# Optimization experiments

Measured on AMD Instinct MI355X. Metric: run time of the kernel, lower is better.

Reference implementation:

```python
import jax, jax.numpy as jnp
import numpy as np

NUM_HEADS = 12


def setup_inputs() -> dict:
    key = jax.random.key(0)
    k0, k1, k2 = jax.random.split(key, 3)
    B, N, C = 32, 864, 768  # N = 2*t_h*t_w + s_h*s_w = 288 + 576
    x = jax.random.normal(k0, (B, N, C), dtype=jnp.float32)
    W_qkv = jax.random.normal(k1, (C, 3 * C), dtype=jnp.float32) * 0.02
    W_proj = jax.random.normal(k2, (C, C), dtype=jnp.float32) * 0.02
    b_proj = jnp.zeros((C,), dtype=jnp.float32)
    return {"x": x, "W_qkv": W_qkv, "W_proj": W_proj, "b_proj": b_proj,
            "t_h": 12, "t_w": 12, "s_h": 24, "s_w": 24}


def reference(x, W_qkv, W_proj, b_proj, t_h, t_w, s_h, s_w):
    B, N, C = x.shape
    H = NUM_HEADS
    d = C // H
    scale = d ** -0.5
    # qkv projection (no bias), shape [3, B, H, N, d]
    qkv = (x @ W_qkv).reshape(B, N, 3, H, d).transpose(2, 0, 3, 1, 4)
    q, k, v = qkv[0], qkv[1], qkv[2]
    Tt = 2 * t_h * t_w            # temporal (template) query tokens = 288
    Ts = s_h * s_w                # spatial (search) query tokens = 576
    Mt = 2 * ((t_h + 1) // 2) ** 2  # sub-sampled temporal kv tokens = 72
    Ms = (s_h * s_w) // 4           # sub-sampled spatial kv tokens = 144
    q_t, q_s = q[:, :, :Tt], q[:, :, Tt:Tt + Ts]
    k_t, k_s = k[:, :, :Mt], k[:, :, Mt:Mt + Ms]
    v_t, v_s = v[:, :, :Mt], v[:, :, Mt:Mt + Ms]
    # temporal queries attend spatial keys/values
    a_t = jax.nn.softmax(jnp.einsum('bhqd,bhkd->bhqk', q_t, k_s) * scale, axis=-1)
    x_t = jnp.einsum('bhqk,bhkd->bhqd', a_t, v_s).transpose(0, 2, 1, 3).reshape(B, Tt, C)
    # spatial queries attend temporal keys/values
    a_s = jax.nn.softmax(jnp.einsum('bhqd,bhkd->bhqk', q_s, k_t) * scale, axis=-1)
    x_s = jnp.einsum('bhqk,bhkd->bhqd', a_s, v_t).transpose(0, 2, 1, 3).reshape(B, Ts, C)
    out = jnp.concatenate([x_t, x_s], axis=1)  # [B, N, C]
    return out @ W_proj + b_proj
```

## Files before the change

kernel.cpp:

```cpp
#include <hip/hip_runtime.h>
#include <hip/hip_bf16.h>

typedef __attribute__((ext_vector_type(8))) short short8;
typedef __attribute__((ext_vector_type(4))) float floatx4;

#define MFMA16(a, b, c) __builtin_amdgcn_mfma_f32_16x16x32_bf16((a), (b), (c), 0, 0, 0)

static constexpr int Bb = 32, Nn = 864, Cc = 768, Hh = 12;
static constexpr int Mm = Bb * Nn;
static constexpr int NKV = 2 * Cc;
static constexpr int KVROWS = 256;

__device__ __forceinline__ void gload_lds16(const __hip_bfloat16* g, __hip_bfloat16* l) {
    __builtin_amdgcn_global_load_lds((const __attribute__((address_space(1))) void*)g,
                                     (__attribute__((address_space(3))) void*)l, 16, 0, 0);
}

static constexpr int CVT_BLKS = (Mm * Cc / 4) / 256;
static constexpr int TQKV_BLKS = (3 * Cc / 32) * (Cc / 32);
static constexpr int TPROJ_BLKS = (Cc / 32) * (Cc / 32);

__global__ __launch_bounds__(256) void prep_kernel(const float* __restrict__ x,
                                                   const float* __restrict__ Wqkv,
                                                   const float* __restrict__ Wproj,
                                                   __hip_bfloat16* __restrict__ xb,
                                                   __hip_bfloat16* __restrict__ WqkvT,
                                                   __hip_bfloat16* __restrict__ WprojT) {
    __shared__ float tile[32][33];
    const int bx = blockIdx.x;
    if (bx < CVT_BLKS) {
        const int i = bx * 256 + threadIdx.x;
        const float4 v = ((const float4*)x)[i];
        __hip_bfloat16 o[4] = {__float2bfloat16(v.x), __float2bfloat16(v.y),
                               __float2bfloat16(v.z), __float2bfloat16(v.w)};
        ((uint2*)xb)[i] = *(const uint2*)o;
        return;
    }
    const float* in;
    __hip_bfloat16* out;
    int R, C, bid;
    if (bx < CVT_BLKS + TQKV_BLKS) {
        bid = bx - CVT_BLKS; in = Wqkv; out = WqkvT; R = Cc; C = 3 * Cc;
    } else {
        bid = bx - CVT_BLKS - TQKV_BLKS; in = Wproj; out = WprojT; R = Cc; C = Cc;
    }
    const int c0 = (bid % (C / 32)) * 32, r0 = (bid / (C / 32)) * 32;
    const int tx = threadIdx.x & 31, ty = threadIdx.x >> 5;
#pragma unroll
    for (int i = 0; i < 32; i += 8)
        tile[ty + i][tx] = in[(size_t)(r0 + ty + i) * C + c0 + tx];
    __syncthreads();
#pragma unroll
    for (int i = 0; i < 32; i += 8)
        out[(size_t)(c0 + ty + i) * R + r0 + tx] = __float2bfloat16(tile[tx][ty + i]);
}

static constexpr int QBLKS = 6 * (Mm / 128);
static constexpr int KVBLKS = 12 * (Bb * KVROWS / 128);
static constexpr int QKV_NWG = QBLKS + KVBLKS;

__global__ __launch_bounds__(256) void gemm_qkv2(const __hip_bfloat16* __restrict__ A,
                                                 const __hip_bfloat16* __restrict__ WqkvT,
                                                 __hip_bfloat16* __restrict__ Qbuf,
                                                 __hip_bfloat16* __restrict__ KVbuf) {
    __shared__ __align__(16) __hip_bfloat16 As[8192];
    __shared__ __align__(16) __hip_bfloat16 Bs[8192];

    const int braw = (int)blockIdx.x;
    const int sid = (braw & 7) * (QKV_NWG / 8) + (braw >> 3);

    int arow0, orow0, btrow0, ncol0, Nout;
    __hip_bfloat16* Out;
    if (sid < QBLKS) {
        const int nt = sid % 6, mt = sid / 6;
        arow0 = mt * 128; orow0 = arow0;
        btrow0 = nt * 128; ncol0 = nt * 128;
        Out = Qbuf; Nout = Cc;
    } else {
        const int s = sid - QBLKS;
        const int nt = s % 12, mt = s / 12;
        const int bb = mt >> 1, keybase = (mt & 1) << 7;
        arow0 = bb * Nn + keybase;
        orow0 = bb * KVROWS + keybase;
        btrow0 = Cc + nt * 128;
        ncol0 = nt * 128;
        Out = KVbuf; Nout = NKV;
    }

    const int t = threadIdx.x;
    const int lane = t & 63, wave = t >> 6;
    const int wm = (wave >> 1) * 64, wn = (wave & 1) * 64;
    const int ln = lane & 15, quad = lane >> 4;

    floatx4 acc[4][4] = {};

    const int r0 = t >> 2;
    const int cst = (t & 3) * 8;
    const __hip_bfloat16* Ag = A + (size_t)(arow0 + r0) * Cc + cst;
    const __hip_bfloat16* Bg = WqkvT + (size_t)(btrow0 + r0) * Cc + cst;
    const size_t rowskip = (size_t)64 * Cc;

    for (int k0 = 0; k0 < Cc; k0 += 64) {
        gload_lds16(Ag + k0,                &As[t * 8]);
        gload_lds16(Ag + k0 + rowskip,      &As[2048 + t * 8]);
        gload_lds16(Ag + k0 + 32,           &As[4096 + t * 8]);
        gload_lds16(Ag + k0 + 32 + rowskip, &As[6144 + t * 8]);
        gload_lds16(Bg + k0,                &Bs[t * 8]);
        gload_lds16(Bg + k0 + rowskip,      &Bs[2048 + t * 8]);
        gload_lds16(Bg + k0 + 32,           &Bs[4096 + t * 8]);
        gload_lds16(Bg + k0 + 32 + rowskip, &Bs[6144 + t * 8]);
        __syncthreads();

#pragma unroll
        for (int s = 0; s < 2; s++) {
            short8 af[4], bfr[4];
#pragma unroll
            for (int i = 0; i < 4; i++)
                af[i] = *(const short8*)&As[s * 4096 + (wm + i * 16 + ln) * 32 + quad * 8];
#pragma unroll
            for (int j = 0; j < 4; j++)
                bfr[j] = *(const short8*)&Bs[s * 4096 + (wn + j * 16 + ln) * 32 + quad * 8];
#pragma unroll
            for (int i = 0; i < 4; i++)
#pragma unroll
                for (int j = 0; j < 4; j++)
                    acc[i][j] = MFMA16(af[i], bfr[j], acc[i][j]);
        }
        __syncthreads();
    }

#pragma unroll
    for (int j = 0; j < 4; j++) {
        const int n = ncol0 + wn + j * 16 + ln;
#pragma unroll
        for (int i = 0; i < 4; i++) {
            const int mrow = orow0 + wm + i * 16 + quad * 4;
#pragma unroll
            for (int r = 0; r < 4; r++)
                Out[(size_t)(mrow + r) * Nout + n] = __float2bfloat16(acc[i][j][r]);
        }
    }
}

__global__ __launch_bounds__(256) void gemm_proj(const __hip_bfloat16* __restrict__ A,
                                                 const __hip_bfloat16* __restrict__ BT,
                                                 float* __restrict__ Cout,
                                                 const float* __restrict__ bias) {
    __shared__ __align__(16) __hip_bfloat16 As[8192];
    __shared__ __align__(16) __hip_bfloat16 Bs[8192];
    const int gx = (int)gridDim.x;
    const int nwg = gx * (int)gridDim.y;
    const int braw = (int)blockIdx.y * gx + (int)blockIdx.x;
    const int sid = (braw & 7) * (nwg >> 3) + (braw >> 3);
    const int mt = sid / gx, nt = sid - mt * gx;
    const int m0 = mt << 7, n0 = nt * 128;
    const int t = threadIdx.x;
    const int lane = t & 63, wave = t >> 6;
    const int wm = (wave >> 1) * 64, wn = (wave & 1) * 64;
    const int ln = lane & 15, quad = lane >> 4;

    floatx4 acc[4][4] = {};
    const int r0 = t >> 2, cst = (t & 3) * 8;
    const __hip_bfloat16* Ag = A + (size_t)(m0 + r0) * Cc + cst;
    const __hip_bfloat16* Bg = BT + (size_t)(n0 + r0) * Cc + cst;
    const size_t rowskip = (size_t)64 * Cc;

    for (int k0 = 0; k0 < Cc; k0 += 64) {
        gload_lds16(Ag + k0,                &As[t * 8]);
        gload_lds16(Ag + k0 + rowskip,      &As[2048 + t * 8]);
        gload_lds16(Ag + k0 + 32,           &As[4096 + t * 8]);
        gload_lds16(Ag + k0 + 32 + rowskip, &As[6144 + t * 8]);
        gload_lds16(Bg + k0,                &Bs[t * 8]);
        gload_lds16(Bg + k0 + rowskip,      &Bs[2048 + t * 8]);
        gload_lds16(Bg + k0 + 32,           &Bs[4096 + t * 8]);
        gload_lds16(Bg + k0 + 32 + rowskip, &Bs[6144 + t * 8]);
        __syncthreads();
#pragma unroll
        for (int s = 0; s < 2; s++) {
            short8 af[4], bfr[4];
#pragma unroll
            for (int i = 0; i < 4; i++)
                af[i] = *(const short8*)&As[s * 4096 + (wm + i * 16 + ln) * 32 + quad * 8];
#pragma unroll
            for (int j = 0; j < 4; j++)
                bfr[j] = *(const short8*)&Bs[s * 4096 + (wn + j * 16 + ln) * 32 + quad * 8];
#pragma unroll
            for (int i = 0; i < 4; i++)
#pragma unroll
                for (int j = 0; j < 4; j++)
                    acc[i][j] = MFMA16(af[i], bfr[j], acc[i][j]);
        }
        __syncthreads();
    }
#pragma unroll
    for (int j = 0; j < 4; j++) {
        const int n = n0 + wn + j * 16 + ln;
        const float bv = bias[n];
#pragma unroll
        for (int i = 0; i < 4; i++) {
            const int mrow = m0 + wm + i * 16 + quad * 4;
#pragma unroll
            for (int r = 0; r < 4; r++)
                Cout[(size_t)(mrow + r) * Cc + n] = acc[i][j][r] + bv;
        }
    }
}

template <int L, int QOFF, int KVOFF, int NQT, int NCH>
__device__ __forceinline__ void attn_pair(const __hip_bfloat16* __restrict__ qb,
                                          const __hip_bfloat16* __restrict__ kv,
                                          __hip_bfloat16* __restrict__ attn,
                                          int qc, int h, int b,
                                          __hip_bfloat16* VTs) {
    constexpr int KPAD = NCH * 32;
    constexpr int VSTR = KPAD + 8;
    constexpr int NPAIR = NQT / 2;
    const int t = threadIdx.x, lane = t & 63, wave = t >> 6;
    const int ln = lane & 15, quad = lane >> 4;
    const __hip_bfloat16 z16 = __float2bfloat16(0.0f);

    const __hip_bfloat16* kbase = kv + (size_t)(b * KVROWS + KVOFF) * NKV + h * 64;
    const __hip_bfloat16* vbase = kbase + Cc;

    for (int c = t; c < KPAD * 8; c += 256) {
        const int key = c >> 3, s8 = c & 7, d0 = s8 * 8;
        const int colp = (key + 8 * s8) % KPAD;
        if (key < L) {
            uint4 raw = *(const uint4*)(vbase + (size_t)key * NKV + d0);
            const __hip_bfloat16* pv = (const __hip_bfloat16*)&raw;
#pragma unroll
            for (int jj = 0; jj < 8; jj++) VTs[(d0 + jj) * VSTR + colp] = pv[jj];
        } else {
#pragma unroll
            for (int jj = 0; jj < 8; jj++) VTs[(d0 + jj) * VSTR + colp] = z16;
        }
    }
    __syncthreads();

    const int pt = qc * 4 + wave;
    if (pt >= NPAIR) return;

    const int qt0 = 2 * pt;
    const __hip_bfloat16* qrowA =
        qb + (size_t)(b * Nn + QOFF + qt0 * 16 + ln) * Cc + h * 64;
    const __hip_bfloat16* qrowB = qrowA + (size_t)16 * Cc;
    const short8 aqA0 = *(const short8*)(qrowA + quad * 8);
    const short8 aqA1 = *(const short8*)(qrowA + 32 + quad * 8);
    const short8 aqB0 = *(const short8*)(qrowB + quad * 8);
    const short8 aqB1 = *(const short8*)(qrowB + 32 + quad * 8);

    float dsA = 0.0f, dsB = 0.0f;
    floatx4 accA[4] = {}, accB[4] = {};
    constexpr float CSC = 0.18033688011112042f;

#pragma unroll
    for (int ch = 0; ch < NCH; ch++) {
        unsigned int pkA[2][2], pkB[2][2];
#pragma unroll
        for (int ti2 = 0; ti2 < 2; ti2++) {
            const int ti = ch * 2 + ti2;
            if (ti * 16 >= L) {
                pkA[ti2][0] = 0u; pkA[ti2][1] = 0u;
                pkB[ti2][0] = 0u; pkB[ti2][1] = 0u;
                continue;
            }
            const __hip_bfloat16* krow = kbase + (size_t)(ti * 16 + ln) * NKV;
            const short8 k0 = *(const short8*)(krow + quad * 8);
            const short8 k1 = *(const short8*)(krow + 32 + quad * 8);
            floatx4 sA = {0.f, 0.f, 0.f, 0.f}, sB = {0.f, 0.f, 0.f, 0.f};
            sA = MFMA16(k0, aqA0, sA);
            sA = MFMA16(k1, aqA1, sA);
            sB = MFMA16(k0, aqB0, sB);
            sB = MFMA16(k1, aqB1, sB);
            float pA[4], pB[4];
#pragma unroll
            for (int r = 0; r < 4; r++) {
                float eA = exp2f(sA[r] * CSC);
                float eB = exp2f(sB[r] * CSC);
                if (ti * 16 + 16 > L) {
                    if (ti * 16 + quad * 4 + r >= L) { eA = 0.0f; eB = 0.0f; }
                }
                pA[r] = eA; dsA += eA;
                pB[r] = eB; dsB += eB;
            }
            {
                const __hip_bfloat162 lo = __float22bfloat162_rn(make_float2(pA[0], pA[1]));
                const __hip_bfloat162 hi = __float22bfloat162_rn(make_float2(pA[2], pA[3]));
                pkA[ti2][0] = *(const unsigned int*)&lo;
                pkA[ti2][1] = *(const unsigned int*)&hi;
            }
            {
                const __hip_bfloat162 lo = __float22bfloat162_rn(make_float2(pB[0], pB[1]));
                const __hip_bfloat162 hi = __float22bfloat162_rn(make_float2(pB[2], pB[3]));
                pkB[ti2][0] = *(const unsigned int*)&lo;
                pkB[ti2][1] = *(const unsigned int*)&hi;
            }
        }
        const int srcA = ln + ((quad & 1) << 5);
        const int srcB = srcA + 16;
        const bool hi2 = quad >= 2;
        union { unsigned int u[4]; short8 v; } pfA, pfB;
        {
            const unsigned int c0 = (unsigned int)__shfl((int)pkA[0][0], srcA);
            const unsigned int c1 = (unsigned int)__shfl((int)pkA[0][1], srcA);
            const unsigned int c2 = (unsigned int)__shfl((int)pkA[0][0], srcB);
            const unsigned int c3 = (unsigned int)__shfl((int)pkA[0][1], srcB);
            const unsigned int d0 = (unsigned int)__shfl((int)pkA[1][0], srcA);
            const unsigned int d1 = (unsigned int)__shfl((int)pkA[1][1], srcA);
            const unsigned int d2 = (unsigned int)__shfl((int)pkA[1][0], srcB);
            const unsigned int d3 = (unsigned int)__shfl((int)pkA[1][1], srcB);
            pfA.u[0] = hi2 ? d0 : c0;
            pfA.u[1] = hi2 ? d1 : c1;
            pfA.u[2] = hi2 ? d2 : c2;
            pfA.u[3] = hi2 ? d3 : c3;
        }
        {
            const unsigned int c0 = (unsigned int)__shfl((int)pkB[0][0], srcA);
            const unsigned int c1 = (unsigned int)__shfl((int)pkB[0][1], srcA);
            const unsigned int c2 = (unsigned int)__shfl((int)pkB[0][0], srcB);
            const unsigned int c3 = (unsigned int)__shfl((int)pkB[0][1], srcB);
            const unsigned int d0 = (unsigned int)__shfl((int)pkB[1][0], srcA);
            const unsigned int d1 = (unsigned int)__shfl((int)pkB[1][1], srcA);
            const unsigned int d2 = (unsigned int)__shfl((int)pkB[1][0], srcB);
            const unsigned int d3 = (unsigned int)__shfl((int)pkB[1][1], srcB);
            pfB.u[0] = hi2 ? d0 : c0;
            pfB.u[1] = hi2 ? d1 : c1;
            pfB.u[2] = hi2 ? d2 : c2;
            pfB.u[3] = hi2 ? d3 : c3;
        }
#pragma unroll
        for (int j = 0; j < 4; j++) {
            const int dd = j * 16 + ln;
            const int colp = (ch * 32 + quad * 8 + ((dd >> 3) << 3)) % KPAD;
            const short8 vt = *(const short8*)&VTs[dd * VSTR + colp];
            accA[j] = MFMA16(vt, pfA.v, accA[j]);
            accB[j] = MFMA16(vt, pfB.v, accB[j]);
        }
    }

    dsA += __shfl_xor(dsA, 16); dsA += __shfl_xor(dsA, 32);
    dsB += __shfl_xor(dsB, 16); dsB += __shfl_xor(dsB, 32);
    const float invA = 1.0f / dsA, invB = 1.0f / dsB;

    const size_t orowA = (size_t)(b * Nn + QOFF + qt0 * 16 + ln) * Cc + h * 64;
    const size_t orowB = orowA + (size_t)16 * Cc;
#pragma unroll
    for (int j = 0; j < 4; j++) {
        {
            const __hip_bfloat162 lo =
                __float22bfloat162_rn(make_float2(accA[j][0] * invA, accA[j][1] * invA));
            const __hip_bfloat162 hi =
                __float22bfloat162_rn(make_float2(accA[j][2] * invA, accA[j][3] * invA));
            uint2 o = make_uint2(*(const unsigned int*)&lo, *(const unsigned int*)&hi);
            *(uint2*)&attn[orowA + j * 16 + quad * 4] = o;
        }
        {
            const __hip_bfloat162 lo =
                __float22bfloat162_rn(make_float2(accB[j][0] * invB, accB[j][1] * invB));
            const __hip_bfloat162 hi =
                __float22bfloat162_rn(make_float2(accB[j][2] * invB, accB[j][3] * invB));
            uint2 o = make_uint2(*(const unsigned int*)&lo, *(const unsigned int*)&hi);
            *(uint2*)&attn[orowB + j * 16 + quad * 4] = o;
        }
    }
}

static constexpr int ATTN_NB = 8 * Hh * Bb;

__global__ __launch_bounds__(256, 4) void attn_fused(const __hip_bfloat16* __restrict__ qb,
                                                     const __hip_bfloat16* __restrict__ kv,
                                                     __hip_bfloat16* __restrict__ attn) {
    __shared__ __align__(16) __hip_bfloat16 VTs[64 * 168];
    const int rid = (int)blockIdx.x + 8 * ((int)blockIdx.y + 12 * (int)blockIdx.z);
    const int vid = (rid & 7) * (ATTN_NB / 8) + (rid >> 3);
    const int qc = vid % 8, g = vid / 8;
    const int h = g % 12, bq = g / 12;
    if (qc < 3)
        attn_pair<144, 0, 72, 18, 5>(qb, kv, attn, qc, h, bq, VTs);
    else
        attn_pair<72, 288, 0, 36, 3>(qb, kv, attn, qc - 3, h, bq, VTs);
}

extern "C" void kernel_launch(void* const* d_in, const int* in_sizes, int n_in,
                              void* d_out, int out_size, void* d_ws, size_t ws_size,
                              hipStream_t stream) {
    const float* x     = (const float*)d_in[0];
    const float* Wqkv  = (const float*)d_in[1];
    const float* Wproj = (const float*)d_in[2];
    const float* bproj = (const float*)d_in[3];
    float* out = (float*)d_out;

    char* ws = (char*)d_ws;
    __hip_bfloat16* xb     = (__hip_bfloat16*)ws;
    __hip_bfloat16* WqkvT  = (__hip_bfloat16*)(ws + 42467328);
    __hip_bfloat16* WprojT = (__hip_bfloat16*)(ws + 46006272);
    __hip_bfloat16* Qbuf   = (__hip_bfloat16*)(ws + 47185920);
    __hip_bfloat16* KVbuf  = (__hip_bfloat16*)(ws + 89653248);
    __hip_bfloat16* attn   = (__hip_bfloat16*)ws;

    prep_kernel<<<CVT_BLKS + TQKV_BLKS + TPROJ_BLKS, 256, 0, stream>>>(x, Wqkv, Wproj, xb,
                                                                       WqkvT, WprojT);
    gemm_qkv2<<<QKV_NWG, 256, 0, stream>>>(xb, WqkvT, Qbuf, KVbuf);
    attn_fused<<<dim3(8, Hh, Bb), 256, 0, stream>>>(Qbuf, KVbuf, attn);
    gemm_proj<<<dim3(Cc / 128, Mm / 128), 256, 0, stream>>>(attn, WprojT, out, bproj);
}
```

Measured before the change: 336.8 us.

## Double-buffer LDS tiles in QKV and projection GEMMs with MFMA priority

Both GEMM kernels switch from one 64-wide K tile per barrier pair to a double-buffered 32-wide K pipeline. The next tile's global-to-LDS loads are issued before computing on the current buffer, so memory latency can overlap with MFMA work, and each iteration needs one barrier instead of two. s_setprio is raised around the MFMA block. In exchange the K step is halved, giving more iterations and barriers in total, and correctness depends on the async LDS loads completing before the barrier.

```diff
diff --git a/kernel.cpp b/kernel.cpp
--- a/kernel.cpp
+++ b/kernel.cpp
@@ -55,6 +55,28 @@
         out[(size_t)(c0 + ty + i) * R + r0 + tx] = __float2bfloat16(tile[tx][ty + i]);
 }
 
+#define GEMM_STAGE(buf, kk)                                          \
+    do {                                                             \
+        gload_lds16(Ag + (kk),           &As[buf][(size_t)t * 8]);   \
+        gload_lds16(Ag + (kk) + rsk,     &As[buf][2048 + (size_t)t * 8]); \
+        gload_lds16(Bg + (kk),           &Bs[buf][(size_t)t * 8]);   \
+        gload_lds16(Bg + (kk) + rsk,     &Bs[buf][2048 + (size_t)t * 8]); \
+    } while (0)
+
+#define GEMM_COMPUTE(buf)                                                          \
+    do {                                                                           \
+        short8 af[4], bfr[4];                                                      \
+        _Pragma("unroll") for (int i = 0; i < 4; i++)                              \
+            af[i] = *(const short8*)&As[buf][(wm + i * 16 + ln) * 32 + quad * 8];  \
+        _Pragma("unroll") for (int j = 0; j < 4; j++)                              \
+            bfr[j] = *(const short8*)&Bs[buf][(wn + j * 16 + ln) * 32 + quad * 8]; \
+        __builtin_amdgcn_s_setprio(1);                                             \
+        _Pragma("unroll") for (int i = 0; i < 4; i++)                              \
+            _Pragma("unroll") for (int j = 0; j < 4; j++)                          \
+                acc[i][j] = MFMA16(af[i], bfr[j], acc[i][j]);                      \
+        __builtin_amdgcn_s_setprio(0);                                             \
+    } while (0)
+
 static constexpr int QBLKS = 6 * (Mm / 128);
 static constexpr int KVBLKS = 12 * (Bb * KVROWS / 128);
 static constexpr int QKV_NWG = QBLKS + KVBLKS;
@@ -63,8 +85,8 @@
                                                  const __hip_bfloat16* __restrict__ WqkvT,
                                                  __hip_bfloat16* __restrict__ Qbuf,
                                                  __hip_bfloat16* __restrict__ KVbuf) {
-    __shared__ __align__(16) __hip_bfloat16 As[8192];
-    __shared__ __align__(16) __hip_bfloat16 Bs[8192];
+    __shared__ __align__(16) __hip_bfloat16 As[2][4096];
+    __shared__ __align__(16) __hip_bfloat16 Bs[2][4096];
 
     const int braw = (int)blockIdx.x;
     const int sid = (braw & 7) * (QKV_NWG / 8) + (braw >> 3);
@@ -94,40 +116,20 @@
 
     floatx4 acc[4][4] = {};
 
-    const int r0 = t >> 2;
-    const int cst = (t & 3) * 8;
-    const __hip_bfloat16* Ag = A + (size_t)(arow0 + r0) * Cc + cst;
-    const __hip_bfloat16* Bg = WqkvT + (size_t)(btrow0 + r0) * Cc + cst;
-    const size_t rowskip = (size_t)64 * Cc;
-
-    for (int k0 = 0; k0 < Cc; k0 += 64) {
-        gload_lds16(Ag + k0,                &As[t * 8]);
-        gload_lds16(Ag + k0 + rowskip,      &As[2048 + t * 8]);
-        gload_lds16(Ag + k0 + 32,           &As[4096 + t * 8]);
-        gload_lds16(Ag + k0 + 32 + rowskip, &As[6144 + t * 8]);
-        gload_lds16(Bg + k0,                &Bs[t * 8]);
-        gload_lds16(Bg + k0 + rowskip,      &Bs[2048 + t * 8]);
-        gload_lds16(Bg + k0 + 32,           &Bs[4096 + t * 8]);
-        gload_lds16(Bg + k0 + 32 + rowskip, &Bs[6144 + t * 8]);
+    const __hip_bfloat16* Ag = A + (size_t)(arow0 + (t >> 2)) * Cc + (t & 3) * 8;
+    const __hip_bfloat16* Bg = WqkvT + (size_t)(btrow0 + (t >> 2)) * Cc + (t & 3) * 8;
+    const size_t rsk = (size_t)64 * Cc;
+
+    GEMM_STAGE(0, 0);
+    __syncthreads();
+    int cur = 0;
+    for (int ks = 0; ks < 23; ks++) {
+        GEMM_STAGE(cur ^ 1, (ks + 1) * 32);
+        GEMM_COMPUTE(cur);
         __syncthreads();
-
-#pragma unroll
-        for (int s = 0; s < 2; s++) {
-            short8 af[4], bfr[4];
-#pragma unroll
-            for (int i = 0; i < 4; i++)
-                af[i] = *(const short8*)&As[s * 4096 + (wm + i * 16 + ln) * 32 + quad * 8];
-#pragma unroll
-            for (int j = 0; j < 4; j++)
-                bfr[j] = *(const short8*)&Bs[s * 4096 + (wn + j * 16 + ln) * 32 + quad * 8];
-#pragma unroll
-            for (int i = 0; i < 4; i++)
-#pragma unroll
-                for (int j = 0; j < 4; j++)
-                    acc[i][j] = MFMA16(af[i], bfr[j], acc[i][j]);
-        }
-        __syncthreads();
-    }
+        cur ^= 1;
+    }
+    GEMM_COMPUTE(cur);
 
 #pragma unroll
     for (int j = 0; j < 4; j++) {
@@ -146,8 +148,8 @@
                                                  const __hip_bfloat16* __restrict__ BT,
                                                  float* __restrict__ Cout,
                                                  const float* __restrict__ bias) {
-    __shared__ __align__(16) __hip_bfloat16 As[8192];
-    __shared__ __align__(16) __hip_bfloat16 Bs[8192];
+    __shared__ __align__(16) __hip_bfloat16 As[2][4096];
+    __shared__ __align__(16) __hip_bfloat16 Bs[2][4096];
     const int gx = (int)gridDim.x;
     const int nwg = gx * (int)gridDim.y;
     const int braw = (int)blockIdx.y * gx + (int)blockIdx.x;
@@ -160,38 +162,21 @@
     const int ln = lane & 15, quad = lane >> 4;
 
     floatx4 acc[4][4] = {};
-    const int r0 = t >> 2, cst = (t & 3) * 8;
-    const __hip_bfloat16* Ag = A + (size_t)(m0 + r0) * Cc + cst;
-    const __hip_bfloat16* Bg = BT + (size_t)(n0 + r0) * Cc + cst;
-    const size_t rowskip = (size_t)64 * Cc;
-
-    for (int k0 = 0; k0 < Cc; k0 += 64) {
-        gload_lds16(Ag + k0,                &As[t * 8]);
-        gload_lds16(Ag + k0 + rowskip,      &As[2048 + t * 8]);
-        gload_lds16(Ag + k0 + 32,           &As[4096 + t * 8]);
-        gload_lds16(Ag + k0 + 32 + rowskip, &As[6144 + t * 8]);
-        gload_lds16(Bg + k0,                &Bs[t * 8]);
-        gload_lds16(Bg + k0 + rowskip,      &Bs[2048 + t * 8]);
-        gload_lds16(Bg + k0 + 32,           &Bs[4096 + t * 8]);
-        gload_lds16(Bg + k0 + 32 + rowskip, &Bs[6144 + t * 8]);
+    const __hip_bfloat16* Ag = A + (size_t)(m0 + (t >> 2)) * Cc + (t & 3) * 8;
+    const __hip_bfloat16* Bg = BT + (size_t)(n0 + (t >> 2)) * Cc + (t & 3) * 8;
+    const size_t rsk = (size_t)64 * Cc;
+
+    GEMM_STAGE(0, 0);
+    __syncthreads();
+    int cur = 0;
+    for (int ks = 0; ks < 23; ks++) {
+        GEMM_STAGE(cur ^ 1, (ks + 1) * 32);
+        GEMM_COMPUTE(cur);
         __syncthreads();
-#pragma unroll
-        for (int s = 0; s < 2; s++) {
-            short8 af[4], bfr[4];
-#pragma unroll
-            for (int i = 0; i < 4; i++)
-                af[i] = *(const short8*)&As[s * 4096 + (wm + i * 16 + ln) * 32 + quad * 8];
-#pragma unroll
-            for (int j = 0; j < 4; j++)
-                bfr[j] = *(const short8*)&Bs[s * 4096 + (wn + j * 16 + ln) * 32 + quad * 8];
-#pragma unroll
-            for (int i = 0; i < 4; i++)
-#pragma unroll
-                for (int j = 0; j < 4; j++)
-                    acc[i][j] = MFMA16(af[i], bfr[j], acc[i][j]);
-        }
-        __syncthreads();
-    }
+        cur ^= 1;
+    }
+    GEMM_COMPUTE(cur);
+
 #pragma unroll
     for (int j = 0; j < 4; j++) {
         const int n = n0 + wn + j * 16 + ln;
```

Result: slower. 345.0 us (+2.4%).
